# Kernel optimization log

Hardware: AMD Instinct MI355X
Metric: run time of the kernel (lower is better)

## Reference

```python
import jax, jax.numpy as jnp
import numpy as np
import math

B, C, FDIM, TP = 32, 64, 128, 32
NHID, NOUT, E, RATIO = 256, 128, 512, 0.8
BN_EPS = 1e-5


def setup_inputs() -> dict:
    key = jax.random.key(0)
    ks = jax.random.split(key, 10)
    nrm = lambda k, shp, s=1.0: jax.random.normal(k, shp, jnp.float32) * s
    return {
        "h": nrm(ks[0], (B, C, FDIM, TP)),
        "edge_index": jax.random.randint(ks[1], (2, E), 0, C, dtype=jnp.int32),
        "edge_weight": jax.random.uniform(ks[2], (E,), jnp.float32),
        "gc1_w": nrm(ks[3], (FDIM, NHID), 1.0 / math.sqrt(FDIM)),
        "gc1_b": jnp.zeros((NHID,), jnp.float32),
        "bn1_gamma": jnp.ones((NHID,), jnp.float32),
        "bn1_beta": jnp.zeros((NHID,), jnp.float32),
        "bn1_mean": jnp.zeros((NHID,), jnp.float32),
        "bn1_var": jnp.ones((NHID,), jnp.float32),
        "prelu1_a": jnp.full((1,), 0.25, jnp.float32),
        "pool1_w": nrm(ks[4], (NHID, 1), 1.0 / math.sqrt(NHID)),
        "pool1_b": jnp.zeros((1,), jnp.float32),
        "gc2_w": nrm(ks[5], (NHID, NOUT), 1.0 / math.sqrt(NHID)),
        "gc2_b": jnp.zeros((NOUT,), jnp.float32),
        "bn2_gamma": jnp.ones((NOUT,), jnp.float32),
        "bn2_beta": jnp.zeros((NOUT,), jnp.float32),
        "bn2_mean": jnp.zeros((NOUT,), jnp.float32),
        "bn2_var": jnp.ones((NOUT,), jnp.float32),
        "prelu2_a": jnp.full((1,), 0.25, jnp.float32),
        "pool2_w": nrm(ks[6], (NOUT, 1), 1.0 / math.sqrt(NOUT)),
        "pool2_b": jnp.zeros((1,), jnp.float32),
    }


def _gcn(x, row, col, w, W, b, n):
    """PyG GCNConv: x @ W, add self-loops (weight 1), symmetric norm, scatter to col, + bias."""
    xw = x @ W
    loop = jnp.arange(n, dtype=row.dtype)
    r = jnp.concatenate([row, loop])
    c = jnp.concatenate([col, loop])
    wf = jnp.concatenate([w, jnp.ones((n,), x.dtype)])
    deg = jax.ops.segment_sum(wf, c, num_segments=n)
    deg_safe = jnp.where(deg > 0, deg, 1.0)
    dis = jnp.where(deg > 0, jax.lax.rsqrt(deg_safe), 0.0)  # deg^-1/2, inf -> 0
    norm = dis[r] * wf * dis[c]
    out = jax.ops.segment_sum(norm[:, None] * xw[r], c, num_segments=n)
    return out + b


def _bn(x, gamma, beta, mean, var):
    return gamma * (x - mean) * jax.lax.rsqrt(var + BN_EPS) + beta


def _prelu(x, a):
    return jnp.where(x >= 0, x, a * x)


def _sagpool(x, row, col, w, valid, Wp, bp, G, N, ratio):
    """SAGPool: GCN score (no edge weights => valid mask as binary weights), per-graph top-k,
    gate by tanh(score), reindex edges (filter_adj via masking). All graphs have N nodes."""
    n = G * N
    score = _gcn(x, row, col, valid.astype(x.dtype), Wp, bp, n)[:, 0]
    k = math.ceil(ratio * N)  # static: uniform graph sizes
    _, idx = jax.lax.top_k(score.reshape(G, N), k)
    perm = (jnp.arange(G, dtype=row.dtype)[:, None] * N + idx.astype(row.dtype)).reshape(-1)
    xk = x[perm] * jnp.tanh(score[perm])[:, None]
    node_map = jnp.full((n,), -1, dtype=row.dtype).at[perm].set(
        jnp.arange(G * k, dtype=row.dtype))
    nr, nc = node_map[row], node_map[col]
    v2 = valid & (nr >= 0) & (nc >= 0)
    nr = jnp.where(v2, nr, 0)
    nc = jnp.where(v2, nc, 0)
    w2 = jnp.where(v2, w, 0.0)
    return xk, nr, nc, w2, v2, k


def _forward(h, edge_index, edge_weight, gc1_w, gc1_b, bn1_gamma, bn1_beta, bn1_mean,
             bn1_var, prelu1_a, pool1_w, pool1_b, gc2_w, gc2_b, bn2_gamma, bn2_beta,
             bn2_mean, bn2_var, prelu2_a, pool2_w, pool2_b):
    b, c, f, tp = h.shape
    G = b * tp
    x = jnp.transpose(h, (0, 3, 1, 2)).reshape(G * c, f)  # fold time into batch of graphs
    offs = jnp.arange(G, dtype=edge_index.dtype) * c
    row = (edge_index[0][None, :] + offs[:, None]).reshape(-1)
    col = (edge_index[1][None, :] + offs[:, None]).reshape(-1)
    w = jnp.tile(edge_weight, G)
    valid = jnp.ones(row.shape, dtype=bool)

    x = _gcn(x, row, col, w, gc1_w, gc1_b, G * c)
    x = _prelu(_bn(x, bn1_gamma, bn1_beta, bn1_mean, bn1_var), prelu1_a)
    x, row, col, w, valid, k1 = _sagpool(x, row, col, w, valid, pool1_w, pool1_b, G, c, RATIO)
    # dropout: eval mode -> identity
    x = _gcn(x, row, col, w, gc2_w, gc2_b, G * k1)
    x = _prelu(_bn(x, bn2_gamma, bn2_beta, bn2_mean, bn2_var), prelu2_a)
    x, row, col, w, valid, k2 = _sagpool(x, row, col, w, valid, pool2_w, pool2_b, G, k1, RATIO)

    z = x.reshape(G, k2, -1).mean(axis=1)  # global_mean_pool (uniform segments)
    z_seq = z.reshape(b, tp, -1)
    return x, z_seq


def reference(h, edge_index, edge_weight, gc1_w, gc1_b, bn1_gamma, bn1_beta, bn1_mean,
              bn1_var, prelu1_a, pool1_w, pool1_b, gc2_w, gc2_b, bn2_gamma, bn2_beta,
              bn2_mean, bn2_var, prelu2_a, pool2_w, pool2_b):
    return _forward(h, edge_index, edge_weight, gc1_w, gc1_b, bn1_gamma, bn1_beta,
                    bn1_mean, bn1_var, prelu1_a, pool1_w, pool1_b, gc2_w, gc2_b,
                    bn2_gamma, bn2_beta, bn2_mean, bn2_var, prelu2_a, pool2_w, pool2_b)
```

## Files before the change

kernel.cpp:

```cpp
#include <hip/hip_runtime.h>
#include <math.h>

#define B_   32
#define C_   64
#define F_   128
#define TP_  32
#define G_   (B_*TP_)
#define NHID 256
#define NOUT 128
#define E_   512
#define K1_  52
#define K2_  42
#define N2_  (G_*K1_)

typedef __attribute__((ext_vector_type(8))) short short8_t;
typedef __attribute__((ext_vector_type(4))) float f32x4_t;

__device__ __forceinline__ void split_bf16(float v, unsigned short &h, unsigned short &l) {
  unsigned u = __float_as_uint(v);
  unsigned hb = (u + 0x7FFFu + ((u >> 16) & 1u)) & 0xFFFF0000u;
  float hf = __uint_as_float(hb);
  float r = v - hf;
  unsigned ur = __float_as_uint(r);
  unsigned lb = (ur + 0x7FFFu + ((ur >> 16) & 1u)) >> 16;
  h = (unsigned short)(hb >> 16);
  l = (unsigned short)lb;
}

__device__ __forceinline__ void split3_bf16(float v, unsigned short &h,
                                            unsigned short &m, unsigned short &l) {
  unsigned u = __float_as_uint(v);
  unsigned hb = (u + 0x7FFFu + ((u >> 16) & 1u)) & 0xFFFF0000u;
  float hf = __uint_as_float(hb);
  float r1 = v - hf;
  unsigned u1 = __float_as_uint(r1);
  unsigned mb = (u1 + 0x7FFFu + ((u1 >> 16) & 1u)) & 0xFFFF0000u;
  float mf = __uint_as_float(mb);
  float r2 = r1 - mf;
  unsigned u2 = __float_as_uint(r2);
  unsigned lb = (u2 + 0x7FFFu + ((u2 >> 16) & 1u)) >> 16;
  h = (unsigned short)(hb >> 16);
  m = (unsigned short)(mb >> 16);
  l = (unsigned short)lb;
}

__global__ __launch_bounds__(256) void build_A1(const int* __restrict__ ei,
                                                const float* __restrict__ ew,
                                                float* __restrict__ A1,
                                                float* __restrict__ As1) {
  __shared__ float A1s[C_*C_], As1s[C_*C_];
  __shared__ float dg[C_], dgs[C_], dis[C_], diss[C_];
  int t = threadIdx.x;
  for (int i = t; i < C_*C_; i += 256) { A1s[i] = 0.f; As1s[i] = 0.f; }
  if (t < C_) { dg[t] = 1.f; dgs[t] = 1.f; }
  int r0[2], c0[2]; float w0[2];
#pragma unroll
  for (int p = 0; p < 2; ++p) {
    int e = t + p*256;
    r0[p] = ei[e]; c0[p] = ei[E_ + e]; w0[p] = ew[e];
  }
  __syncthreads();
#pragma unroll
  for (int p = 0; p < 2; ++p) {
    atomicAdd(&dg[c0[p]], w0[p]);
    atomicAdd(&dgs[c0[p]], 1.f);
  }
  __syncthreads();
  if (t < C_) { dis[t] = rsqrtf(dg[t]); diss[t] = rsqrtf(dgs[t]); }
  __syncthreads();
#pragma unroll
  for (int p = 0; p < 2; ++p) {
    int r = r0[p], c = c0[p];
    atomicAdd(&A1s[c*C_ + r],  dis[r] * w0[p] * dis[c]);
    atomicAdd(&As1s[c*C_ + r], diss[r] * diss[c]);
  }
  if (t < C_) {
    atomicAdd(&A1s[t*C_ + t],  dis[t] * dis[t]);
    atomicAdd(&As1s[t*C_ + t], diss[t] * diss[t]);
  }
  __syncthreads();
  for (int i = t; i < C_*C_; i += 256) { A1[i] = A1s[i]; As1[i] = As1s[i]; }
}

__global__ __launch_bounds__(256) void w1prep(const float* __restrict__ W1,
                                              unsigned short* __restrict__ Whi,
                                              unsigned short* __restrict__ Wlo) {
  int tid = blockIdx.x*256 + threadIdx.x;
  int col = tid >> 6, k2 = tid & 63;
  float v0 = W1[(size_t)(2*k2)*NHID + col];
  float v1 = W1[(size_t)(2*k2+1)*NHID + col];
  unsigned short h0,l0,h1,l1;
  split_bf16(v0, h0, l0);
  split_bf16(v1, h1, l1);
  *(unsigned*)&Whi[(size_t)col*128 + 2*k2] = (unsigned)h0 | ((unsigned)h1 << 16);
  *(unsigned*)&Wlo[(size_t)col*128 + 2*k2] = (unsigned)l0 | ((unsigned)l1 << 16);
}

__global__ __launch_bounds__(256) void w2prep(const float* __restrict__ W2,
                                              unsigned short* __restrict__ Whi,
                                              unsigned short* __restrict__ Wmid,
                                              unsigned short* __restrict__ Wlo) {
  int tid = blockIdx.x*256 + threadIdx.x;
  int col = tid >> 7, k2 = tid & 127;
  float v0 = W2[(size_t)(2*k2)*NOUT + col];
  float v1 = W2[(size_t)(2*k2+1)*NOUT + col];
  unsigned short h0,m0,l0,h1,m1,l1;
  split3_bf16(v0, h0, m0, l0);
  split3_bf16(v1, h1, m1, l1);
  *(unsigned*)&Whi [(size_t)col*256 + 2*k2] = (unsigned)h0 | ((unsigned)h1 << 16);
  *(unsigned*)&Wmid[(size_t)col*256 + 2*k2] = (unsigned)m0 | ((unsigned)m1 << 16);
  *(unsigned*)&Wlo [(size_t)col*256 + 2*k2] = (unsigned)l0 | ((unsigned)l1 << 16);
}

__global__ __launch_bounds__(256) void preagg_b(const float* __restrict__ h,
                                                const float* __restrict__ A1,
                                                float* __restrict__ xa2) {
  int bid = blockIdx.x; int b = bid >> 5, q = bid & 31;
  __shared__ float At[64*68];
  __shared__ __align__(16) float Hs[64*132];
  int t = threadIdx.x;
#pragma unroll
  for (int p = 0; p < 16; ++p) {
    int m = t + p*256;
    At[(m & 63)*68 + (m >> 6)] = A1[m];
  }
  const float* hb = h + ((size_t)b*64)*4096 + q*128;
#pragma unroll
  for (int p = 0; p < 8; ++p) {
    int idx = t + p*256;
    int j = idx >> 5, f4 = idx & 31;
    *(float4*)&Hs[j*132 + f4*4] = *(const float4*)(hb + (size_t)j*4096 + f4*4);
  }
  __syncthreads();
  int tx = t & 31, ty = t >> 5;
  float acc[8][4] = {};
  for (int j = 0; j < 64; ++j) {
    float a[8];
    *(float4*)&a[0] = *(const float4*)&At[j*68 + ty*8];
    *(float4*)&a[4] = *(const float4*)&At[j*68 + ty*8 + 4];
    float4 hv = *(const float4*)&Hs[j*132 + tx*4];
#pragma unroll
    for (int i = 0; i < 8; ++i) {
      acc[i][0] = fmaf(a[i], hv.x, acc[i][0]);
      acc[i][1] = fmaf(a[i], hv.y, acc[i][1]);
      acc[i][2] = fmaf(a[i], hv.z, acc[i][2]);
      acc[i][3] = fmaf(a[i], hv.w, acc[i][3]);
    }
  }
  float* outp = xa2 + (((size_t)b*64) << 12) + q*128 + tx*4;
#pragma unroll
  for (int i = 0; i < 8; ++i) {
    int c = ty*8 + i;
    *(float4*)(outp + ((size_t)c << 12)) =
        make_float4(acc[i][0], acc[i][1], acc[i][2], acc[i][3]);
  }
}

__global__ __launch_bounds__(256) void xa_cvt(const float* __restrict__ xa2,
                                              unsigned short* __restrict__ xahi,
                                              unsigned short* __restrict__ xalo) {
  int bid = blockIdx.x;
  int b = bid >> 5, c0 = (bid & 31) * 2;
  __shared__ float xs[8192];
  int t = threadIdx.x;
  const float* src = xa2 + ((size_t)(b*64 + c0) << 12);
#pragma unroll
  for (int p = 0; p < 8; ++p) {
    int idx = (t + p*256) * 4;
    *(float4*)&xs[idx] = *(const float4*)(src + idx);
  }
  __syncthreads();
  int row_l = t >> 2, fq = t & 3;
  int c_l = row_l >> 5, tp = row_l & 31;
  size_t R = ((size_t)b*32 + tp)*64 + c0 + c_l;
  const float* base = &xs[c_l*4096 + tp];
#pragma unroll
  for (int i = 0; i < 4; ++i) {
    int f8 = fq + 4*i;
    unsigned hp[4], lp[4];
#pragma unroll
    for (int jj = 0; jj < 4; ++jj) {
      unsigned short h0,l0,h1,l1;
      split_bf16(base[(f8*8 + 2*jj    )*32], h0, l0);
      split_bf16(base[(f8*8 + 2*jj + 1)*32], h1, l1);
      hp[jj] = (unsigned)h0 | ((unsigned)h1 << 16);
      lp[jj] = (unsigned)l0 | ((unsigned)l1 << 16);
    }
    *(uint4*)&xahi[R*128 + f8*8] = make_uint4(hp[0], hp[1], hp[2], hp[3]);
    *(uint4*)&xalo[R*128 + f8*8] = make_uint4(lp[0], lp[1], lp[2], lp[3]);
  }
}

__global__ __launch_bounds__(256) void gemm1m(const unsigned short* __restrict__ xahi,
                                              const unsigned short* __restrict__ xalo,
                                              const unsigned short* __restrict__ Whi,
                                              const unsigned short* __restrict__ Wlo,
                                              const float* __restrict__ gc1b,
                                              const float* __restrict__ g1,
                                              const float* __restrict__ be1,
                                              const float* __restrict__ mu1,
                                              const float* __restrict__ v1,
                                              const float* __restrict__ pa1,
                                              const float* __restrict__ pw1,
                                              float* __restrict__ y1,
                                              float* __restrict__ dots2) {
  __shared__ unsigned short Ahs[64*40], Als[64*40];
  __shared__ unsigned short Bhs[128*40], Bls[128*40];
  __shared__ float dsum[64*4];
  int t = threadIdx.x;
  int row0 = blockIdx.x * 64;
  int colhalf = blockIdx.y;
  int w = t >> 6, l = t & 63, lr = l & 15, lg = l >> 4;
  f32x4_t acc[4][2] = {};
  for (int k0 = 0; k0 < 128; k0 += 32) {
    {
      int row = t >> 2, kq = t & 3;
      size_t src = (size_t)(row0 + row)*128 + k0 + kq*8;
      *(uint4*)&Ahs[row*40 + kq*8] = *(const uint4*)&xahi[src];
      *(uint4*)&Als[row*40 + kq*8] = *(const uint4*)&xalo[src];
    }
#pragma unroll
    for (int p = 0; p < 2; ++p) {
      int id = t + p*256;
      int colb = id >> 2, kq = id & 3;
      size_t src = (size_t)(colhalf*128 + colb)*128 + k0 + kq*8;
      *(uint4*)&Bhs[colb*40 + kq*8] = *(const uint4*)&Whi[src];
      *(uint4*)&Bls[colb*40 + kq*8] = *(const uint4*)&Wlo[src];
    }
    __syncthreads();
    short8_t ah[4], al[4], bh[2], bl[2];
#pragma unroll
    for (int s = 0; s < 4; ++s) {
      int off = (s*16 + lr)*40 + lg*8;
      ah[s] = *(const short8_t*)&Ahs[off];
      al[s] = *(const short8_t*)&Als[off];
    }
#pragma unroll
    for (int t2 = 0; t2 < 2; ++t2) {
      int off = (w*32 + t2*16 + lr)*40 + lg*8;
      bh[t2] = *(const short8_t*)&Bhs[off];
      bl[t2] = *(const short8_t*)&Bls[off];
    }
#pragma unroll
    for (int s = 0; s < 4; ++s)
#pragma unroll
      for (int t2 = 0; t2 < 2; ++t2) {
        acc[s][t2] = __builtin_amdgcn_mfma_f32_16x16x32_bf16(ah[s], bh[t2], acc[s][t2], 0, 0, 0);
        acc[s][t2] = __builtin_amdgcn_mfma_f32_16x16x32_bf16(al[s], bh[t2], acc[s][t2], 0, 0, 0);
        acc[s][t2] = __builtin_amdgcn_mfma_f32_16x16x32_bf16(ah[s], bl[t2], acc[s][t2], 0, 0, 0);
      }
    __syncthreads();
  }
  float sc_[2], sh_[2], pw_[2];
#pragma unroll
  for (int t2 = 0; t2 < 2; ++t2) {
    int col_g = colhalf*128 + w*32 + t2*16 + lr;
    float s = g1[col_g] * rsqrtf(v1[col_g] + 1e-5f);
    sc_[t2] = s;
    sh_[t2] = (gc1b[col_g] - mu1[col_g])*s + be1[col_g];
    pw_[t2] = pw1[col_g];
  }
  float a1v = pa1[0];
#pragma unroll
  for (int s = 0; s < 4; ++s)
#pragma unroll
    for (int j = 0; j < 4; ++j) {
      int row_l = s*16 + lg*4 + j;
      size_t R = (size_t)row0 + row_l;
      float d = 0.f;
#pragma unroll
      for (int t2 = 0; t2 < 2; ++t2) {
        float o = acc[s][t2][j]*sc_[t2] + sh_[t2];
        o = o >= 0.f ? o : a1v*o;
        y1[R*NHID + colhalf*128 + w*32 + t2*16 + lr] = o;
        d += o * pw_[t2];
      }
      d += __shfl_xor(d, 1);
      d += __shfl_xor(d, 2);
      d += __shfl_xor(d, 4);
      d += __shfl_xor(d, 8);
      if (lr == 0) dsum[row_l*4 + w] = d;
    }
  __syncthreads();
  if (t < 64)
    dots2[((size_t)row0 + t)*2 + colhalf] =
        (dsum[t*4+0] + dsum[t*4+1]) + (dsum[t*4+2] + dsum[t*4+3]);
}

__global__ __launch_bounds__(256) void pool1s(const float* __restrict__ dots2,
                                              const float* __restrict__ As1,
                                              const float* __restrict__ p1b,
                                              int* __restrict__ rowsrc,
                                              float* __restrict__ rowgate,
                                              int* __restrict__ nidx) {
  int g = blockIdx.x, t = threadIdx.x;
  __shared__ float As1s[64*65];
  __shared__ float sp[64], s[64];
  __shared__ int perm[K1_];
  __shared__ float gate[K1_];
  for (int i = t; i < 4096; i += 256)
    As1s[(i >> 6)*65 + (i & 63)] = As1[i];
  if (t < 64) sp[t] = dots2[(g*64 + t)*2] + dots2[(g*64 + t)*2 + 1];
  __syncthreads();
  if (t < 64) {
    float acc = p1b[0];
    for (int j = 0; j < 64; ++j) acc = fmaf(As1s[t*65 + j], sp[j], acc);
    s[t] = acc;
  }
  __syncthreads();
  if (t < 64) {
    float si = s[t];
    int rank = 0;
    for (int j = 0; j < 64; ++j) {
      float sj = s[j];
      rank += (sj > si) || (sj == si && j < t);
    }
    nidx[g*64 + t] = (rank < K1_) ? rank : -1;
    if (rank < K1_) { perm[rank] = t; gate[rank] = tanhf(si); }
  }
  __syncthreads();
  if (t < K1_) {
    rowsrc[g*K1_ + t]  = g*64 + perm[t];
    rowgate[g*K1_ + t] = gate[t];
  }
}

__global__ __launch_bounds__(256) void gemm2m(const float* __restrict__ y1,
                                              const int* __restrict__ rowsrc,
                                              const unsigned short* __restrict__ Whi,
                                              const unsigned short* __restrict__ Wmid,
                                              const unsigned short* __restrict__ Wlo,
                                              float* __restrict__ xw2) {
  __shared__ unsigned short Ahs[64*40], Ams[64*40], Als[64*40];
  __shared__ unsigned short Bhs[128*40], Bms[128*40], Bls[128*40];
  int t = threadIdx.x;
  int row0 = blockIdx.x * 64;
  int w = t >> 6, l = t & 63, lr = l & 15, lg = l >> 4;
  int arow = t >> 2, akq = t & 3;
  size_t asrc = (size_t)rowsrc[row0 + arow] * NHID;
  f32x4_t acc[4][2] = {};
  for (int k0 = 0; k0 < NHID; k0 += 32) {
    {
      const float* src = y1 + asrc + k0 + akq*8;
      float4 v0 = *(const float4*)(src);
      float4 v1 = *(const float4*)(src + 4);
      float e[8] = {v0.x, v0.y, v0.z, v0.w, v1.x, v1.y, v1.z, v1.w};
      unsigned hq[4], mq[4], lq[4];
#pragma unroll
      for (int jj = 0; jj < 4; ++jj) {
        unsigned short h0,m0,l0,h1,m1,l1;
        split3_bf16(e[2*jj],   h0, m0, l0);
        split3_bf16(e[2*jj+1], h1, m1, l1);
        hq[jj] = (unsigned)h0 | ((unsigned)h1 << 16);
        mq[jj] = (unsigned)m0 | ((unsigned)m1 << 16);
        lq[jj] = (unsigned)l0 | ((unsigned)l1 << 16);
      }
      *(uint4*)&Ahs[arow*40 + akq*8] = make_uint4(hq[0], hq[1], hq[2], hq[3]);
      *(uint4*)&Ams[arow*40 + akq*8] = make_uint4(mq[0], mq[1], mq[2], mq[3]);
      *(uint4*)&Als[arow*40 + akq*8] = make_uint4(lq[0], lq[1], lq[2], lq[3]);
    }
#pragma unroll
    for (int p = 0; p < 2; ++p) {
      int id = t + p*256;
      int colb = id >> 2, kq = id & 3;
      size_t src = (size_t)colb*256 + k0 + kq*8;
      *(uint4*)&Bhs[colb*40 + kq*8] = *(const uint4*)&Whi[src];
      *(uint4*)&Bms[colb*40 + kq*8] = *(const uint4*)&Wmid[src];
      *(uint4*)&Bls[colb*40 + kq*8] = *(const uint4*)&Wlo[src];
    }
    __syncthreads();
    short8_t ah[4], am[4], al[4], bh[2], bm[2], bl[2];
#pragma unroll
    for (int s = 0; s < 4; ++s) {
      int off = (s*16 + lr)*40 + lg*8;
      ah[s] = *(const short8_t*)&Ahs[off];
      am[s] = *(const short8_t*)&Ams[off];
      al[s] = *(const short8_t*)&Als[off];
    }
#pragma unroll
    for (int t2 = 0; t2 < 2; ++t2) {
      int off = (w*32 + t2*16 + lr)*40 + lg*8;
      bh[t2] = *(const short8_t*)&Bhs[off];
      bm[t2] = *(const short8_t*)&Bms[off];
      bl[t2] = *(const short8_t*)&Bls[off];
    }
#pragma unroll
    for (int s = 0; s < 4; ++s)
#pragma unroll
      for (int t2 = 0; t2 < 2; ++t2) {
        acc[s][t2] = __builtin_amdgcn_mfma_f32_16x16x32_bf16(ah[s], bh[t2], acc[s][t2], 0, 0, 0);
        acc[s][t2] = __builtin_amdgcn_mfma_f32_16x16x32_bf16(ah[s], bm[t2], acc[s][t2], 0, 0, 0);
        acc[s][t2] = __builtin_amdgcn_mfma_f32_16x16x32_bf16(am[s], bh[t2], acc[s][t2], 0, 0, 0);
        acc[s][t2] = __builtin_amdgcn_mfma_f32_16x16x32_bf16(ah[s], bl[t2], acc[s][t2], 0, 0, 0);
        acc[s][t2] = __builtin_amdgcn_mfma_f32_16x16x32_bf16(am[s], bm[t2], acc[s][t2], 0, 0, 0);
        acc[s][t2] = __builtin_amdgcn_mfma_f32_16x16x32_bf16(al[s], bh[t2], acc[s][t2], 0, 0, 0);
      }
    __syncthreads();
  }
#pragma unroll
  for (int s = 0; s < 4; ++s)
#pragma unroll
    for (int t2 = 0; t2 < 2; ++t2)
#pragma unroll
      for (int j = 0; j < 4; ++j) {
        int row_l = s*16 + lg*4 + j;
        int col = w*32 + t2*16 + lr;
        xw2[(size_t)(row0 + row_l)*NOUT + col] = acc[s][t2][j];
      }
}

__global__ __launch_bounds__(256) void mega2r(const int* __restrict__ ei,
                                              const float* __restrict__ ew,
                                              const int* __restrict__ nidx,
                                              const float* __restrict__ xw2,
                                              const float* __restrict__ rowgate,
                                              const float* __restrict__ gc2b,
                                              const float* __restrict__ g2,
                                              const float* __restrict__ be2,
                                              const float* __restrict__ mu2,
                                              const float* __restrict__ v2,
                                              const float* __restrict__ pa2,
                                              const float* __restrict__ pw2,
                                              const float* __restrict__ p2b,
                                              float* __restrict__ out) {
  int g = blockIdx.x, t = threadIdx.x;
  __shared__ float A2t[64*68];
  __shared__ float As2s[K1_*K1_];
  __shared__ __align__(16) float xs[K1_*132];
  __shared__ float dg[K1_], dgs[K1_], dis[K1_], diss[K1_], d[K1_], s[K1_], gA[K1_];
  __shared__ int nm[C_], rankA[K1_];
  __shared__ float4 zpart[8][32];

  for (int i = t; i < 64*68; i += 256) A2t[i] = 0.f;
  for (int i = t; i < K1_*K1_; i += 256) As2s[i] = 0.f;
  if (t < C_) nm[t] = nidx[g*C_ + t];
  if (t < K1_) { dg[t] = 1.f; dgs[t] = 1.f; }
  for (int p = 0; p < 7; ++p) {
    int idx = t + p*256;
    if (idx < K1_*32) {
      int r = idx >> 5, f4 = idx & 31;
      float gt = rowgate[g*K1_ + r];
      float4 v = *(const float4*)(xw2 + ((size_t)g*K1_ + r)*NOUT + f4*4);
      v.x *= gt; v.y *= gt; v.z *= gt; v.w *= gt;
      *(float4*)&xs[r*132 + f4*4] = v;
    }
  }
  int eR[2], eC[2]; float eW[2];
#pragma unroll
  for (int p = 0; p < 2; ++p) {
    int e = t + p*256;
    eR[p] = ei[e]; eC[p] = ei[E_ + e]; eW[p] = ew[e];
  }
  __syncthreads();
  int nr[2], nc[2]; bool val[2];
#pragma unroll
  for (int p = 0; p < 2; ++p) {
    nr[p] = nm[eR[p]]; nc[p] = nm[eC[p]];
    val[p] = (nr[p] >= 0) && (nc[p] >= 0);
    if (val[p]) { atomicAdd(&dg[nc[p]], eW[p]); atomicAdd(&dgs[nc[p]], 1.f); }
  }
  __syncthreads();
  if (t < K1_) { dis[t] = rsqrtf(dg[t]); diss[t] = rsqrtf(dgs[t]); }
  __syncthreads();
#pragma unroll
  for (int p = 0; p < 2; ++p) {
    if (val[p]) {
      atomicAdd(&A2t[nr[p]*68 + nc[p]],  dis[nr[p]] * eW[p] * dis[nc[p]]);
      atomicAdd(&As2s[nc[p]*K1_ + nr[p]], diss[nr[p]] * diss[nc[p]]);
    }
  }
  if (t < K1_) {
    atomicAdd(&A2t[t*68 + t],   dis[t]*dis[t]);
    atomicAdd(&As2s[t*K1_ + t], diss[t]*diss[t]);
  }
  __syncthreads();
  int tx = t & 31, ty = t >> 5;
  float4 scv, shv, pwv;
  {
    int col = 4*tx;
    float4 gv = *(const float4*)(g2 + col);
    float4 vv = *(const float4*)(v2 + col);
    float4 bv = *(const float4*)(be2 + col);
    float4 mv = *(const float4*)(mu2 + col);
    float4 b0 = *(const float4*)(gc2b + col);
    scv.x = gv.x * rsqrtf(vv.x + 1e-5f); scv.y = gv.y * rsqrtf(vv.y + 1e-5f);
    scv.z = gv.z * rsqrtf(vv.z + 1e-5f); scv.w = gv.w * rsqrtf(vv.w + 1e-5f);
    shv = make_float4((b0.x - mv.x)*scv.x + bv.x, (b0.y - mv.y)*scv.y + bv.y,
                      (b0.z - mv.z)*scv.z + bv.z, (b0.w - mv.w)*scv.w + bv.w);
    pwv = *(const float4*)(pw2 + col);
  }
  float a2v = pa2[0];
  float acc[8][4] = {};
  for (int j = 0; j < K1_; ++j) {
    float a[8];
    *(float4*)&a[0] = *(const float4*)&A2t[j*68 + ty*8];
    *(float4*)&a[4] = *(const float4*)&A2t[j*68 + ty*8 + 4];
    float4 xv = *(const float4*)&xs[j*132 + tx*4];
#pragma unroll
    for (int i = 0; i < 8; ++i) {
      acc[i][0] = fmaf(a[i], xv.x, acc[i][0]);
      acc[i][1] = fmaf(a[i], xv.y, acc[i][1]);
      acc[i][2] = fmaf(a[i], xv.z, acc[i][2]);
      acc[i][3] = fmaf(a[i], xv.w, acc[i][3]);
    }
  }
#pragma unroll
  for (int i = 0; i < 8; ++i) {
    int c = ty*8 + i;
    if (c < K1_) {
      float4 o;
      o.x = acc[i][0]*scv.x + shv.x; o.y = acc[i][1]*scv.y + shv.y;
      o.z = acc[i][2]*scv.z + shv.z; o.w = acc[i][3]*scv.w + shv.w;
      o.x = o.x >= 0.f ? o.x : a2v*o.x; o.y = o.y >= 0.f ? o.y : a2v*o.y;
      o.z = o.z >= 0.f ? o.z : a2v*o.z; o.w = o.w >= 0.f ? o.w : a2v*o.w;
      acc[i][0] = o.x; acc[i][1] = o.y; acc[i][2] = o.z; acc[i][3] = o.w;
      float dp = o.x*pwv.x + o.y*pwv.y + o.z*pwv.z + o.w*pwv.w;
      dp += __shfl_xor(dp, 1);
      dp += __shfl_xor(dp, 2);
      dp += __shfl_xor(dp, 4);
      dp += __shfl_xor(dp, 8);
      dp += __shfl_xor(dp, 16);
      if (tx == 0) d[c] = dp;
    }
  }
  __syncthreads();
  if (t < K1_) {
    float sv = p2b[0];
    for (int j = 0; j < K1_; ++j) sv = fmaf(As2s[t*K1_ + j], d[j], sv);
    s[t] = sv;
  }
  __syncthreads();
  if (t < K1_) {
    float si = s[t];
    int rank = 0;
    for (int j = 0; j < K1_; ++j) {
      float sj = s[j];
      rank += (sj > si) || (sj == si && j < t);
    }
    rankA[t] = rank;
    gA[t] = tanhf(si);
  }
  __syncthreads();
  float4 zp = make_float4(0.f, 0.f, 0.f, 0.f);
#pragma unroll
  for (int i = 0; i < 8; ++i) {
    int c = ty*8 + i;
    if (c < K1_) {
      int r = rankA[c];
      if (r < K2_) {
        float gt = gA[c];
        float4 v = make_float4(acc[i][0]*gt, acc[i][1]*gt, acc[i][2]*gt, acc[i][3]*gt);
        *(float4*)(out + ((size_t)g*K2_ + r)*NOUT + 4*tx) = v;
        zp.x += v.x; zp.y += v.y; zp.z += v.z; zp.w += v.w;
      }
    }
  }
  zpart[ty][tx] = zp;
  __syncthreads();
  if (t < 32) {
    float4 z = make_float4(0.f, 0.f, 0.f, 0.f);
#pragma unroll
    for (int k = 0; k < 8; ++k) {
      float4 v = zpart[k][t];
      z.x += v.x; z.y += v.y; z.z += v.z; z.w += v.w;
    }
    const float inv = 1.0f / (float)K2_;
    z.x *= inv; z.y *= inv; z.z *= inv; z.w *= inv;
    *(float4*)(out + (size_t)G_*K2_*NOUT + (size_t)g*NOUT + 4*t) = z;
  }
}

extern "C" void kernel_launch(void* const* d_in, const int* in_sizes, int n_in,
                              void* d_out, int out_size, void* d_ws, size_t ws_size,
                              hipStream_t stream) {
  const float* h    = (const float*)d_in[0];
  const int*   ei   = (const int*)  d_in[1];
  const float* ew   = (const float*)d_in[2];
  const float* gc1w = (const float*)d_in[3];
  const float* gc1b = (const float*)d_in[4];
  const float* bn1g = (const float*)d_in[5];
  const float* bn1b = (const float*)d_in[6];
  const float* bn1m = (const float*)d_in[7];
  const float* bn1v = (const float*)d_in[8];
  const float* pr1a = (const float*)d_in[9];
  const float* p1w  = (const float*)d_in[10];
  const float* p1b  = (const float*)d_in[11];
  const float* gc2w = (const float*)d_in[12];
  const float* gc2b = (const float*)d_in[13];
  const float* bn2g = (const float*)d_in[14];
  const float* bn2b = (const float*)d_in[15];
  const float* bn2m = (const float*)d_in[16];
  const float* bn2v = (const float*)d_in[17];
  const float* pr2a = (const float*)d_in[18];
  const float* p2w  = (const float*)d_in[19];
  const float* p2b  = (const float*)d_in[20];

  float* w = (float*)d_ws;
  float*          A1      = w;
  float*          As1     = w + 4096;
  float*          dots2   = w + 8192;
  int*            nidx    = (int*)(w + 139264);
  int*            rowsrc  = (int*)(w + 204800);
  float*          rowgate = w + 258048;
  unsigned short* W1thi   = (unsigned short*)(w + 311296);
  unsigned short* W1tlo   = (unsigned short*)(w + 327680);
  unsigned short* W2thi   = (unsigned short*)(w + 344064);
  unsigned short* W2tmid  = (unsigned short*)(w + 360448);
  unsigned short* W2tlo   = (unsigned short*)(w + 376832);
  float*          xa2     = w + 393216;
  unsigned short* xahi    = (unsigned short*)(w + 8781824);
  unsigned short* xalo    = (unsigned short*)(w + 12976128);
  float*          y1      = w + 17170432;
  float*          xw2     = xa2;

  build_A1<<<1, 256, 0, stream>>>(ei, ew, A1, As1);
  w1prep<<<64, 256, 0, stream>>>(gc1w, W1thi, W1tlo);
  w2prep<<<64, 256, 0, stream>>>(gc2w, W2thi, W2tmid, W2tlo);
  preagg_b<<<1024, 256, 0, stream>>>(h, A1, xa2);
  xa_cvt<<<1024, 256, 0, stream>>>(xa2, xahi, xalo);
  gemm1m<<<dim3(1024, 2), 256, 0, stream>>>(xahi, xalo, W1thi, W1tlo, gc1b,
                                            bn1g, bn1b, bn1m, bn1v, pr1a, p1w,
                                            y1, dots2);
  pool1s<<<G_, 256, 0, stream>>>(dots2, As1, p1b, rowsrc, rowgate, nidx);
  gemm2m<<<832, 256, 0, stream>>>(y1, rowsrc, W2thi, W2tmid, W2tlo, xw2);
  mega2r<<<G_, 256, 0, stream>>>(ei, ew, nidx, xw2, rowgate, gc2b, bn2g, bn2b,
                                 bn2m, bn2v, pr2a, p2w, p2b, (float*)d_out);
}
```

Before: 147.7 us.

## Fuse second GCN GEMM into per-graph aggregation/pool kernel

Merges the gemm2m MFMA GEMM into the per-graph mega kernel, so each block computes its graph's 52 gated rows of x@W2 directly into shared memory instead of writing and re-reading an xw2 buffer through global memory. The gate multiply moves before the bf16 split, and shared memory is aliased across phases with an extra barrier before zpart reuse. It saves one launch and the global round trip. In exchange, 64-row tiles hold only 52 valid rows, so some MFMA work is wasted, and the larger shared footprint may reduce occupancy.

```diff
diff --git a/kernel.cpp b/kernel.cpp
--- a/kernel.cpp
+++ b/kernel.cpp
@@ -11,7 +11,6 @@
 #define E_   512
 #define K1_  52
 #define K2_  42
-#define N2_  (G_*K1_)
 
 typedef __attribute__((ext_vector_type(8))) short short8_t;
 typedef __attribute__((ext_vector_type(4))) float f32x4_t;
@@ -325,95 +324,15 @@
   }
 }
 
-__global__ __launch_bounds__(256) void gemm2m(const float* __restrict__ y1,
+__global__ __launch_bounds__(256) void mega2f(const float* __restrict__ y1,
                                               const int* __restrict__ rowsrc,
+                                              const float* __restrict__ rowgate,
                                               const unsigned short* __restrict__ Whi,
                                               const unsigned short* __restrict__ Wmid,
                                               const unsigned short* __restrict__ Wlo,
-                                              float* __restrict__ xw2) {
-  __shared__ unsigned short Ahs[64*40], Ams[64*40], Als[64*40];
-  __shared__ unsigned short Bhs[128*40], Bms[128*40], Bls[128*40];
-  int t = threadIdx.x;
-  int row0 = blockIdx.x * 64;
-  int w = t >> 6, l = t & 63, lr = l & 15, lg = l >> 4;
-  int arow = t >> 2, akq = t & 3;
-  size_t asrc = (size_t)rowsrc[row0 + arow] * NHID;
-  f32x4_t acc[4][2] = {};
-  for (int k0 = 0; k0 < NHID; k0 += 32) {
-    {
-      const float* src = y1 + asrc + k0 + akq*8;
-      float4 v0 = *(const float4*)(src);
-      float4 v1 = *(const float4*)(src + 4);
-      float e[8] = {v0.x, v0.y, v0.z, v0.w, v1.x, v1.y, v1.z, v1.w};
-      unsigned hq[4], mq[4], lq[4];
-#pragma unroll
-      for (int jj = 0; jj < 4; ++jj) {
-        unsigned short h0,m0,l0,h1,m1,l1;
-        split3_bf16(e[2*jj],   h0, m0, l0);
-        split3_bf16(e[2*jj+1], h1, m1, l1);
-        hq[jj] = (unsigned)h0 | ((unsigned)h1 << 16);
-        mq[jj] = (unsigned)m0 | ((unsigned)m1 << 16);
-        lq[jj] = (unsigned)l0 | ((unsigned)l1 << 16);
-      }
-      *(uint4*)&Ahs[arow*40 + akq*8] = make_uint4(hq[0], hq[1], hq[2], hq[3]);
-      *(uint4*)&Ams[arow*40 + akq*8] = make_uint4(mq[0], mq[1], mq[2], mq[3]);
-      *(uint4*)&Als[arow*40 + akq*8] = make_uint4(lq[0], lq[1], lq[2], lq[3]);
-    }
-#pragma unroll
-    for (int p = 0; p < 2; ++p) {
-      int id = t + p*256;
-      int colb = id >> 2, kq = id & 3;
-      size_t src = (size_t)colb*256 + k0 + kq*8;
-      *(uint4*)&Bhs[colb*40 + kq*8] = *(const uint4*)&Whi[src];
-      *(uint4*)&Bms[colb*40 + kq*8] = *(const uint4*)&Wmid[src];
-      *(uint4*)&Bls[colb*40 + kq*8] = *(const uint4*)&Wlo[src];
-    }
-    __syncthreads();
-    short8_t ah[4], am[4], al[4], bh[2], bm[2], bl[2];
-#pragma unroll
-    for (int s = 0; s < 4; ++s) {
-      int off = (s*16 + lr)*40 + lg*8;
-      ah[s] = *(const short8_t*)&Ahs[off];
-      am[s] = *(const short8_t*)&Ams[off];
-      al[s] = *(const short8_t*)&Als[off];
-    }
-#pragma unroll
-    for (int t2 = 0; t2 < 2; ++t2) {
-      int off = (w*32 + t2*16 + lr)*40 + lg*8;
-      bh[t2] = *(const short8_t*)&Bhs[off];
-      bm[t2] = *(const short8_t*)&Bms[off];
-      bl[t2] = *(const short8_t*)&Bls[off];
-    }
-#pragma unroll
-    for (int s = 0; s < 4; ++s)
-#pragma unroll
-      for (int t2 = 0; t2 < 2; ++t2) {
-        acc[s][t2] = __builtin_amdgcn_mfma_f32_16x16x32_bf16(ah[s], bh[t2], acc[s][t2], 0, 0, 0);
-        acc[s][t2] = __builtin_amdgcn_mfma_f32_16x16x32_bf16(ah[s], bm[t2], acc[s][t2], 0, 0, 0);
-        acc[s][t2] = __builtin_amdgcn_mfma_f32_16x16x32_bf16(am[s], bh[t2], acc[s][t2], 0, 0, 0);
-        acc[s][t2] = __builtin_amdgcn_mfma_f32_16x16x32_bf16(ah[s], bl[t2], acc[s][t2], 0, 0, 0);
-        acc[s][t2] = __builtin_amdgcn_mfma_f32_16x16x32_bf16(am[s], bm[t2], acc[s][t2], 0, 0, 0);
-        acc[s][t2] = __builtin_amdgcn_mfma_f32_16x16x32_bf16(al[s], bh[t2], acc[s][t2], 0, 0, 0);
-      }
-    __syncthreads();
-  }
-#pragma unroll
-  for (int s = 0; s < 4; ++s)
-#pragma unroll
-    for (int t2 = 0; t2 < 2; ++t2)
-#pragma unroll
-      for (int j = 0; j < 4; ++j) {
-        int row_l = s*16 + lg*4 + j;
-        int col = w*32 + t2*16 + lr;
-        xw2[(size_t)(row0 + row_l)*NOUT + col] = acc[s][t2][j];
-      }
-}
-
-__global__ __launch_bounds__(256) void mega2r(const int* __restrict__ ei,
+                                              const int* __restrict__ ei,
                                               const float* __restrict__ ew,
                                               const int* __restrict__ nidx,
-                                              const float* __restrict__ xw2,
-                                              const float* __restrict__ rowgate,
                                               const float* __restrict__ gc2b,
                                               const float* __restrict__ g2,
                                               const float* __restrict__ be2,
@@ -423,28 +342,99 @@
                                               const float* __restrict__ pw2,
                                               const float* __restrict__ p2b,
                                               float* __restrict__ out) {
-  int g = blockIdx.x, t = threadIdx.x;
-  __shared__ float A2t[64*68];
-  __shared__ float As2s[K1_*K1_];
-  __shared__ __align__(16) float xs[K1_*132];
+  __shared__ __align__(16) char pool[51584];
+  unsigned short* Ahs = (unsigned short*)(pool);
+  unsigned short* Ams = (unsigned short*)(pool + 5120);
+  unsigned short* Als = (unsigned short*)(pool + 10240);
+  unsigned short* Bhs = (unsigned short*)(pool + 15360);
+  unsigned short* Bms = (unsigned short*)(pool + 25600);
+  unsigned short* Bls = (unsigned short*)(pool + 35840);
+  float* xs   = (float*)(pool);
+  float* A2t  = (float*)(pool + 27456);
+  float* As2s = (float*)(pool + 40768);
+  float4* zpart = (float4*)(pool);
   __shared__ float dg[K1_], dgs[K1_], dis[K1_], diss[K1_], d[K1_], s[K1_], gA[K1_];
   __shared__ int nm[C_], rankA[K1_];
-  __shared__ float4 zpart[8][32];
-
-  for (int i = t; i < 64*68; i += 256) A2t[i] = 0.f;
+
+  int t = threadIdx.x, g = blockIdx.x;
+  int w = t >> 6, l = t & 63, lr = l & 15, lg = l >> 4;
+  int arow = t >> 2, akq = t & 3;
+  int ar = (arow < K1_) ? arow : 0;
+  size_t asrc = (size_t)rowsrc[g*K1_ + ar] * NHID;
+  float gt = rowgate[g*K1_ + ar];
+  f32x4_t macc[4][2] = {};
+  for (int k0 = 0; k0 < NHID; k0 += 32) {
+    {
+      const float* src = y1 + asrc + k0 + akq*8;
+      float4 v0 = *(const float4*)(src);
+      float4 v1 = *(const float4*)(src + 4);
+      float e[8] = {v0.x, v0.y, v0.z, v0.w, v1.x, v1.y, v1.z, v1.w};
+      unsigned hq[4], mq[4], lq[4];
+#pragma unroll
+      for (int jj = 0; jj < 4; ++jj) {
+        unsigned short h0,m0,l0,h1,m1,l1;
+        split3_bf16(gt * e[2*jj],   h0, m0, l0);
+        split3_bf16(gt * e[2*jj+1], h1, m1, l1);
+        hq[jj] = (unsigned)h0 | ((unsigned)h1 << 16);
+        mq[jj] = (unsigned)m0 | ((unsigned)m1 << 16);
+        lq[jj] = (unsigned)l0 | ((unsigned)l1 << 16);
+      }
+      *(uint4*)&Ahs[arow*40 + akq*8] = make_uint4(hq[0], hq[1], hq[2], hq[3]);
+      *(uint4*)&Ams[arow*40 + akq*8] = make_uint4(mq[0], mq[1], mq[2], mq[3]);
+      *(uint4*)&Als[arow*40 + akq*8] = make_uint4(lq[0], lq[1], lq[2], lq[3]);
+    }
+#pragma unroll
+    for (int p = 0; p < 2; ++p) {
+      int id = t + p*256;
+      int colb = id >> 2, kq = id & 3;
+      size_t src = (size_t)colb*256 + k0 + kq*8;
+      *(uint4*)&Bhs[colb*40 + kq*8] = *(const uint4*)&Whi[src];
+      *(uint4*)&Bms[colb*40 + kq*8] = *(const uint4*)&Wmid[src];
+      *(uint4*)&Bls[colb*40 + kq*8] = *(const uint4*)&Wlo[src];
+    }
+    __syncthreads();
+    short8_t ah[4], am[4], al[4], bh[2], bm[2], bl[2];
+#pragma unroll
+    for (int ss = 0; ss < 4; ++ss) {
+      int off = (ss*16 + lr)*40 + lg*8;
+      ah[ss] = *(const short8_t*)&Ahs[off];
+      am[ss] = *(const short8_t*)&Ams[off];
+      al[ss] = *(const short8_t*)&Als[off];
+    }
+#pragma unroll
+    for (int t2 = 0; t2 < 2; ++t2) {
+      int off = (w*32 + t2*16 + lr)*40 + lg*8;
+      bh[t2] = *(const short8_t*)&Bhs[off];
+      bm[t2] = *(const short8_t*)&Bms[off];
+      bl[t2] = *(const short8_t*)&Bls[off];
+    }
+#pragma unroll
+    for (int ss = 0; ss < 4; ++ss)
+#pragma unroll
+      for (int t2 = 0; t2 < 2; ++t2) {
+        macc[ss][t2] = __builtin_amdgcn_mfma_f32_16x16x32_bf16(ah[ss], bh[t2], macc[ss][t2], 0, 0, 0);
+        macc[ss][t2] = __builtin_amdgcn_mfma_f32_16x16x32_bf16(ah[ss], bm[t2], macc[ss][t2], 0, 0, 0);
+        macc[ss][t2] = __builtin_amdgcn_mfma_f32_16x16x32_bf16(am[ss], bh[t2], macc[ss][t2], 0, 0, 0);
+        macc[ss][t2] = __builtin_amdgcn_mfma_f32_16x16x32_bf16(ah[ss], bl[t2], macc[ss][t2], 0, 0, 0);
+        macc[ss][t2] = __builtin_amdgcn_mfma_f32_16x16x32_bf16(am[ss], bm[t2], macc[ss][t2], 0, 0, 0);
+        macc[ss][t2] = __builtin_amdgcn_mfma_f32_16x16x32_bf16(al[ss], bh[t2], macc[ss][t2], 0, 0, 0);
+      }
+    __syncthreads();
+  }
+#pragma unroll
+  for (int ss = 0; ss < 4; ++ss)
+#pragma unroll
+    for (int t2 = 0; t2 < 2; ++t2)
+#pragma unroll
+      for (int j = 0; j < 4; ++j) {
+        int row_l = ss*16 + lg*4 + j;
+        if (row_l < K1_)
+          xs[row_l*132 + w*32 + t2*16 + lr] = macc[ss][t2][j];
+      }
+  for (int i = t; i < K1_*64; i += 256) A2t[i] = 0.f;
   for (int i = t; i < K1_*K1_; i += 256) As2s[i] = 0.f;
   if (t < C_) nm[t] = nidx[g*C_ + t];
   if (t < K1_) { dg[t] = 1.f; dgs[t] = 1.f; }
-  for (int p = 0; p < 7; ++p) {
-    int idx = t + p*256;
-    if (idx < K1_*32) {
-      int r = idx >> 5, f4 = idx & 31;
-      float gt = rowgate[g*K1_ + r];
-      float4 v = *(const float4*)(xw2 + ((size_t)g*K1_ + r)*NOUT + f4*4);
-      v.x *= gt; v.y *= gt; v.z *= gt; v.w *= gt;
-      *(float4*)&xs[r*132 + f4*4] = v;
-    }
-  }
   int eR[2], eC[2]; float eW[2];
 #pragma unroll
   for (int p = 0; p < 2; ++p) {
@@ -465,12 +455,12 @@
 #pragma unroll
   for (int p = 0; p < 2; ++p) {
     if (val[p]) {
-      atomicAdd(&A2t[nr[p]*68 + nc[p]],  dis[nr[p]] * eW[p] * dis[nc[p]]);
+      atomicAdd(&A2t[nr[p]*64 + nc[p]],   dis[nr[p]] * eW[p] * dis[nc[p]]);
       atomicAdd(&As2s[nc[p]*K1_ + nr[p]], diss[nr[p]] * diss[nc[p]]);
     }
   }
   if (t < K1_) {
-    atomicAdd(&A2t[t*68 + t],   dis[t]*dis[t]);
+    atomicAdd(&A2t[t*64 + t],   dis[t]*dis[t]);
     atomicAdd(&As2s[t*K1_ + t], diss[t]*diss[t]);
   }
   __syncthreads();
@@ -490,18 +480,18 @@
     pwv = *(const float4*)(pw2 + col);
   }
   float a2v = pa2[0];
-  float acc[8][4] = {};
+  float aacc[8][4] = {};
   for (int j = 0; j < K1_; ++j) {
     float a[8];
-    *(float4*)&a[0] = *(const float4*)&A2t[j*68 + ty*8];
-    *(float4*)&a[4] = *(const float4*)&A2t[j*68 + ty*8 + 4];
+    *(float4*)&a[0] = *(const float4*)&A2t[j*64 + ty*8];
+    *(float4*)&a[4] = *(const float4*)&A2t[j*64 + ty*8 + 4];
     float4 xv = *(const float4*)&xs[j*132 + tx*4];
 #pragma unroll
     for (int i = 0; i < 8; ++i) {
-      acc[i][0] = fmaf(a[i], xv.x, acc[i][0]);
-      acc[i][1] = fmaf(a[i], xv.y, acc[i][1]);
-      acc[i][2] = fmaf(a[i], xv.z, acc[i][2]);
-      acc[i][3] = fmaf(a[i], xv.w, acc[i][3]);
+      aacc[i][0] = fmaf(a[i], xv.x, aacc[i][0]);
+      aacc[i][1] = fmaf(a[i], xv.y, aacc[i][1]);
+      aacc[i][2] = fmaf(a[i], xv.z, aacc[i][2]);
+      aacc[i][3] = fmaf(a[i], xv.w, aacc[i][3]);
     }
   }
 #pragma unroll
@@ -509,11 +499,11 @@
     int c = ty*8 + i;
     if (c < K1_) {
       float4 o;
-      o.x = acc[i][0]*scv.x + shv.x; o.y = acc[i][1]*scv.y + shv.y;
-      o.z = acc[i][2]*scv.z + shv.z; o.w = acc[i][3]*scv.w + shv.w;
+      o.x = aacc[i][0]*scv.x + shv.x; o.y = aacc[i][1]*scv.y + shv.y;
+      o.z = aacc[i][2]*scv.z + shv.z; o.w = aacc[i][3]*scv.w + shv.w;
       o.x = o.x >= 0.f ? o.x : a2v*o.x; o.y = o.y >= 0.f ? o.y : a2v*o.y;
       o.z = o.z >= 0.f ? o.z : a2v*o.z; o.w = o.w >= 0.f ? o.w : a2v*o.w;
-      acc[i][0] = o.x; acc[i][1] = o.y; acc[i][2] = o.z; acc[i][3] = o.w;
+      aacc[i][0] = o.x; aacc[i][1] = o.y; aacc[i][2] = o.z; aacc[i][3] = o.w;
       float dp = o.x*pwv.x + o.y*pwv.y + o.z*pwv.z + o.w*pwv.w;
       dp += __shfl_xor(dp, 1);
       dp += __shfl_xor(dp, 2);
@@ -548,20 +538,21 @@
     if (c < K1_) {
       int r = rankA[c];
       if (r < K2_) {
-        float gt = gA[c];
-        float4 v = make_float4(acc[i][0]*gt, acc[i][1]*gt, acc[i][2]*gt, acc[i][3]*gt);
+        float gv = gA[c];
+        float4 v = make_float4(aacc[i][0]*gv, aacc[i][1]*gv, aacc[i][2]*gv, aacc[i][3]*gv);
         *(float4*)(out + ((size_t)g*K2_ + r)*NOUT + 4*tx) = v;
         zp.x += v.x; zp.y += v.y; zp.z += v.z; zp.w += v.w;
       }
     }
   }
-  zpart[ty][tx] = zp;
+  __syncthreads();
+  zpart[ty*32 + tx] = zp;
   __syncthreads();
   if (t < 32) {
     float4 z = make_float4(0.f, 0.f, 0.f, 0.f);
 #pragma unroll
     for (int k = 0; k < 8; ++k) {
-      float4 v = zpart[k][t];
+      float4 v = zpart[k*32 + t];
       z.x += v.x; z.y += v.y; z.z += v.z; z.w += v.w;
     }
     const float inv = 1.0f / (float)K2_;
@@ -611,7 +602,6 @@
   unsigned short* xahi    = (unsigned short*)(w + 8781824);
   unsigned short* xalo    = (unsigned short*)(w + 12976128);
   float*          y1      = w + 17170432;
-  float*          xw2     = xa2;
 
   build_A1<<<1, 256, 0, stream>>>(ei, ew, A1, As1);
   w1prep<<<64, 256, 0, stream>>>(gc1w, W1thi, W1tlo);
@@ -622,7 +612,7 @@
                                             bn1g, bn1b, bn1m, bn1v, pr1a, p1w,
                                             y1, dots2);
   pool1s<<<G_, 256, 0, stream>>>(dots2, As1, p1b, rowsrc, rowgate, nidx);
-  gemm2m<<<832, 256, 0, stream>>>(y1, rowsrc, W2thi, W2tmid, W2tlo, xw2);
-  mega2r<<<G_, 256, 0, stream>>>(ei, ew, nidx, xw2, rowgate, gc2b, bn2g, bn2b,
-                                 bn2m, bn2v, pr2a, p2w, p2b, (float*)d_out);
-}
+  mega2f<<<G_, 256, 0, stream>>>(y1, rowsrc, rowgate, W2thi, W2tmid, W2tlo,
+                                 ei, ew, nidx, gc2b, bn2g, bn2b, bn2m, bn2v,
+                                 pr2a, p2w, p2b, (float*)d_out);
+}
```

Result: faster. 138.3 us (-6.4%).
